# Performance work log

Hardware: AMD Instinct MI355X
Metric: run time of the kernel (lower is better)

## Reference

```python
import jax, jax.numpy as jnp
import numpy as np

VOCAB = 32000
D_MODEL = 1024
BLOCK = 2048
RESIDUAL_SCALE = 0.125
B, T = 2, 2048


def setup_inputs() -> dict:
    key = jax.random.key(0)
    ks = jax.random.split(key, 10)
    s = 0.02
    idx = jax.random.randint(ks[0], (B, T), 0, VOCAB)
    tok_emb = jax.random.normal(ks[1], (VOCAB, D_MODEL), jnp.float32) * s
    pos_emb = jax.random.normal(ks[2], (BLOCK, D_MODEL), jnp.float32) * s
    Wq = jax.random.normal(ks[3], (D_MODEL, D_MODEL), jnp.float32) * s
    Wk = jax.random.normal(ks[4], (D_MODEL, D_MODEL), jnp.float32) * s
    Wv = jax.random.normal(ks[5], (D_MODEL, D_MODEL), jnp.float32) * s
    W1 = jax.random.normal(ks[6], (D_MODEL, 4 * D_MODEL), jnp.float32) * s
    b1 = jnp.zeros((4 * D_MODEL,), jnp.float32)
    W2 = jax.random.normal(ks[7], (4 * D_MODEL, D_MODEL), jnp.float32) * s
    b2 = jnp.zeros((D_MODEL,), jnp.float32)
    Wout = jax.random.normal(ks[8], (D_MODEL, VOCAB), jnp.float32) * s
    bout = jnp.zeros((VOCAB,), jnp.float32)
    return {"idx": idx, "tok_emb": tok_emb, "pos_emb": pos_emb, "Wq": Wq,
            "Wk": Wk, "Wv": Wv, "W1": W1, "b1": b1, "W2": W2, "b2": b2,
            "Wout": Wout, "bout": bout}


def reference(idx, tok_emb, pos_emb, Wq, Wk, Wv, W1, b1, W2, b2, Wout, bout):
    Bc, Tc = idx.shape
    scale = 1.0 / jnp.sqrt(jnp.asarray(D_MODEL, jnp.float32))
    x = tok_emb[idx] + pos_emb[:Tc]                       # [B,T,D]
    q = x @ Wq
    k = x @ Wk
    v = x @ Wv
    scores = jnp.einsum('bqd,bkd->bqk', q, k) * scale     # [B,T,T]
    causal = jnp.tril(jnp.ones((Tc, Tc), bool))
    scores = jnp.where(causal, scores, -jnp.inf)
    attn = jax.nn.softmax(scores, axis=-1)
    attn_out = jnp.einsum('bqk,bkd->bqd', attn, v)
    x = x + RESIDUAL_SCALE * attn_out
    h = jax.nn.gelu(x @ W1 + b1, approximate=False)
    x = x + (h @ W2 + b2)
    return x @ Wout + bout                                 # [B,T,V]
```

## Files before the change

### kernel.cpp

```cpp
#include <hip/hip_runtime.h>
#include <math.h>

typedef unsigned int uint;
typedef unsigned short u16;
typedef __bf16 v8bf __attribute__((ext_vector_type(8)));
typedef float v4f __attribute__((ext_vector_type(4)));

__device__ inline u16 f2b(float f) {
  union { float f; uint u; } c; c.f = f;
  uint u = c.u;
  return (u16)((u + 0x7fffu + ((u >> 16) & 1u)) >> 16);
}

__global__ __launch_bounds__(256) void k_embed(
    const int* __restrict__ idx, const float* __restrict__ tok,
    const float* __restrict__ pos, float* __restrict__ x,
    u16* __restrict__ xb, int T, int D) {
  const int r = blockIdx.x;
  const int t = threadIdx.x;
  const int token = idx[r];
  const int p = r % T;
  const float4 a = ((const float4*)(tok + (size_t)token * D))[t];
  const float4 b = ((const float4*)(pos + (size_t)p * D))[t];
  float4 o;
  o.x = a.x + b.x; o.y = a.y + b.y; o.z = a.z + b.z; o.w = a.w + b.w;
  ((float4*)(x + (size_t)r * D))[t] = o;
  ushort4 ob;
  ob.x = f2b(o.x); ob.y = f2b(o.y); ob.z = f2b(o.z); ob.w = f2b(o.w);
  ((ushort4*)(xb + (size_t)r * D))[t] = ob;
}

__global__ __launch_bounds__(256) void k_castT(
    const float* __restrict__ in, u16* __restrict__ out, int R, int C) {
  __shared__ float tile[32][33];
  const int tx = threadIdx.x & 31, ty = threadIdx.x >> 5;
  const int c0 = blockIdx.x * 32, r0 = blockIdx.y * 32;
  for (int j = ty; j < 32; j += 8)
    tile[j][tx] = in[(size_t)(r0 + j) * C + c0 + tx];
  __syncthreads();
  for (int j = ty; j < 32; j += 8)
    out[(size_t)(c0 + j) * R + r0 + tx] = f2b(tile[tx][j]);
}

__global__ __launch_bounds__(256) void k_softmax(
    const float* __restrict__ scores, u16* __restrict__ probs, int T) {
  const int r = blockIdx.x;
  const int i = r % T;
  const float* srow = scores + (size_t)r * T;
  u16* prow = probs + (size_t)r * T;
  const int t = threadIdx.x;
  const int n = i + 1;
  __shared__ float red[256];
  float mx = -3.0e38f;
  for (int j = t; j < n; j += 256) mx = fmaxf(mx, srow[j]);
  red[t] = mx; __syncthreads();
  for (int s = 128; s > 0; s >>= 1) {
    if (t < s) red[t] = fmaxf(red[t], red[t + s]);
    __syncthreads();
  }
  mx = red[0]; __syncthreads();
  float sum = 0.f;
  for (int j = t; j < n; j += 256) sum += __expf(srow[j] - mx);
  red[t] = sum; __syncthreads();
  for (int s = 128; s > 0; s >>= 1) {
    if (t < s) red[t] += red[t + s];
    __syncthreads();
  }
  const float inv = 1.0f / red[0];
  for (int j = t; j < T; j += 256) {
    float p = (j < n) ? __expf(srow[j] - mx) * inv : 0.0f;
    prow[j] = f2b(p);
  }
}

__global__ __launch_bounds__(256) void k_gemm_nt(
    const u16* __restrict__ A, const u16* __restrict__ B,
    const float* __restrict__ src, const float* __restrict__ bias,
    float* __restrict__ Cf, u16* __restrict__ Cb,
    int M, int N, int K, float alpha, int act, int causal_skip) {
  __shared__ __align__(16) u16 As[128 * 40];
  __shared__ __align__(16) u16 Bs[128 * 40];
  const int t = threadIdx.x;
  const int m0 = blockIdx.y * 128, n0 = blockIdx.x * 128;
  if (causal_skip && n0 > m0 + 127) return;
  const int lane = t & 63, wave = t >> 6;
  const int wm = (wave >> 1) * 64, wn = (wave & 1) * 64;
  const int lm = lane & 15, lq = lane >> 4;

  v4f acc[4][4];
#pragma unroll
  for (int i = 0; i < 4; i++)
#pragma unroll
    for (int j = 0; j < 4; j++)
#pragma unroll
      for (int r = 0; r < 4; r++) acc[i][j][r] = 0.0f;

  const int r0 = t >> 2;
  const int cg = (t & 3) * 8;

  for (int k0 = 0; k0 < K; k0 += 32) {
    {
      const size_t abase = (size_t)(m0 + r0) * K + k0 + cg;
      *(uint4*)&As[r0 * 40 + cg]        = *(const uint4*)&A[abase];
      *(uint4*)&As[(r0 + 64) * 40 + cg] = *(const uint4*)&A[abase + (size_t)64 * K];
      const size_t bbase = (size_t)(n0 + r0) * K + k0 + cg;
      *(uint4*)&Bs[r0 * 40 + cg]        = *(const uint4*)&B[bbase];
      *(uint4*)&Bs[(r0 + 64) * 40 + cg] = *(const uint4*)&B[bbase + (size_t)64 * K];
    }
    __syncthreads();
    v8bf af[4], bf[4];
#pragma unroll
    for (int i = 0; i < 4; i++)
      af[i] = *(const v8bf*)&As[(wm + i * 16 + lm) * 40 + lq * 8];
#pragma unroll
    for (int j = 0; j < 4; j++)
      bf[j] = *(const v8bf*)&Bs[(wn + j * 16 + lm) * 40 + lq * 8];
#pragma unroll
    for (int i = 0; i < 4; i++)
#pragma unroll
      for (int j = 0; j < 4; j++)
        acc[i][j] = __builtin_amdgcn_mfma_f32_16x16x32_bf16(af[i], bf[j], acc[i][j], 0, 0, 0);
    __syncthreads();
  }

#pragma unroll
  for (int i = 0; i < 4; i++) {
#pragma unroll
    for (int j = 0; j < 4; j++) {
      const int col = n0 + wn + j * 16 + lm;
      const float bv = bias ? bias[col] : 0.0f;
      const int rowb = m0 + wm + i * 16 + lq * 4;
#pragma unroll
      for (int r = 0; r < 4; r++) {
        float v = alpha * acc[i][j][r] + bv;
        const size_t off = (size_t)(rowb + r) * N + col;
        if (src) v += src[off];
        if (act) v = 0.5f * v * (1.0f + erff(v * 0.70710678118654752f));
        if (Cf) Cf[off] = v;
        if (Cb) Cb[off] = f2b(v);
      }
    }
  }
}

extern "C" void kernel_launch(void* const* d_in, const int* in_sizes, int n_in,
                              void* d_out, int out_size, void* d_ws, size_t ws_size,
                              hipStream_t stream) {
  (void)in_sizes; (void)n_in; (void)out_size; (void)ws_size;
  const int B = 2, T = 2048, D = 1024, V = 32000, H = 4096, M = B * T;
  const int* idx   = (const int*)d_in[0];
  const float* tok = (const float*)d_in[1];
  const float* pos = (const float*)d_in[2];
  const float* Wq  = (const float*)d_in[3];
  const float* Wk  = (const float*)d_in[4];
  const float* Wv  = (const float*)d_in[5];
  const float* W1  = (const float*)d_in[6];
  const float* b1  = (const float*)d_in[7];
  const float* W2  = (const float*)d_in[8];
  const float* b2  = (const float*)d_in[9];
  const float* Wout = (const float*)d_in[10];
  const float* bout = (const float*)d_in[11];
  float* out = (float*)d_out;

  char* w = (char*)d_ws;
  const size_t MB = 1u << 20;
  float* x      = (float*)(w);
  u16*  xb      = (u16*)(w + 16 * MB);
  u16*  qb      = (u16*)(w + 24 * MB);
  u16*  kb      = (u16*)(w + 32 * MB);
  u16*  vt      = (u16*)(w + 40 * MB);
  float* vf     = (float*)(w + 48 * MB);
  float* x2     = vf;
  float* scores = (float*)(w + 64 * MB);
  u16*  hb      = (u16*)(w + 64 * MB);
  u16*  probs   = (u16*)(w + 96 * MB);
  u16*  x2b     = (u16*)(w + 112 * MB);
  u16*  x3b     = (u16*)(w + 120 * MB);
  u16*  wT      = (u16*)(w + 128 * MB);

  dim3 blk(256);

  k_embed<<<M, blk, 0, stream>>>(idx, tok, pos, x, xb, T, D);

  k_castT<<<dim3(D / 32, D / 32), blk, 0, stream>>>(Wq, wT, D, D);
  k_gemm_nt<<<dim3(D / 128, M / 128), blk, 0, stream>>>(
      xb, wT, nullptr, nullptr, nullptr, qb, M, D, D, 1.0f, 0, 0);
  k_castT<<<dim3(D / 32, D / 32), blk, 0, stream>>>(Wk, wT, D, D);
  k_gemm_nt<<<dim3(D / 128, M / 128), blk, 0, stream>>>(
      xb, wT, nullptr, nullptr, nullptr, kb, M, D, D, 1.0f, 0, 0);
  k_castT<<<dim3(D / 32, D / 32), blk, 0, stream>>>(Wv, wT, D, D);
  k_gemm_nt<<<dim3(D / 128, M / 128), blk, 0, stream>>>(
      xb, wT, nullptr, nullptr, vf, nullptr, M, D, D, 1.0f, 0, 0);

  for (int b = 0; b < B; b++)
    k_castT<<<dim3(D / 32, T / 32), blk, 0, stream>>>(
        vf + (size_t)b * T * D, vt + (size_t)b * D * T, T, D);

  for (int b = 0; b < B; b++)
    k_gemm_nt<<<dim3(T / 128, T / 128), blk, 0, stream>>>(
        qb + (size_t)b * T * D, kb + (size_t)b * T * D, nullptr, nullptr,
        scores + (size_t)b * T * T, nullptr, T, T, D, 1.0f / 32.0f, 0, 1);

  k_softmax<<<B * T, blk, 0, stream>>>(scores, probs, T);

  for (int b = 0; b < B; b++)
    k_gemm_nt<<<dim3(D / 128, T / 128), blk, 0, stream>>>(
        probs + (size_t)b * T * T, vt + (size_t)b * D * T,
        x + (size_t)b * T * D, nullptr,
        x2 + (size_t)b * T * D, x2b + (size_t)b * T * D, T, D, T, 0.125f, 0, 0);

  k_castT<<<dim3(H / 32, D / 32), blk, 0, stream>>>(W1, wT, D, H);
  k_gemm_nt<<<dim3(H / 128, M / 128), blk, 0, stream>>>(
      x2b, wT, nullptr, b1, nullptr, hb, M, H, D, 1.0f, 1, 0);

  k_castT<<<dim3(D / 32, H / 32), blk, 0, stream>>>(W2, wT, H, D);
  k_gemm_nt<<<dim3(D / 128, M / 128), blk, 0, stream>>>(
      hb, wT, x2, b2, nullptr, x3b, M, D, H, 1.0f, 0, 0);

  k_castT<<<dim3(V / 32, D / 32), blk, 0, stream>>>(Wout, wT, D, V);
  k_gemm_nt<<<dim3(V / 128, M / 128), blk, 0, stream>>>(
      x3b, wT, nullptr, bout, out, nullptr, M, V, D, 1.0f, 0, 0);
}
```

Before: 1.566 ms.

## Use direct global-to-LDS loads in GEMM, swizzle block order, register-cache softmax

The GEMM tile loads now use global_load_lds, which writes global data straight into LDS without a pass through registers. To fit that path the LDS padding is removed, so rows go from a 40-element to a 32-element stride. Thread blocks are remapped with an XCD-style interleave for better cache locality across the chiplets. Softmax keeps each row's scores in registers so it reads global memory once, instead of re-reading for max, sum and output. The unpadded LDS layout risks bank conflicts on the fragment reads. The softmax hard-codes 8 chunks of 256 elements, which assumes T is at most 2048.

```diff
diff --git a/kernel.cpp b/kernel.cpp
--- a/kernel.cpp
+++ b/kernel.cpp
@@ -5,6 +5,9 @@
 typedef unsigned short u16;
 typedef __bf16 v8bf __attribute__((ext_vector_type(8)));
 typedef float v4f __attribute__((ext_vector_type(4)));
+
+#define GLP(x) ((const __attribute__((address_space(1))) void*)(x))
+#define LDP(x) ((__attribute__((address_space(3))) void*)(x))
 
 __device__ inline u16 f2b(float f) {
   union { float f; uint u; } c; c.f = f;
@@ -51,8 +54,16 @@
   const int t = threadIdx.x;
   const int n = i + 1;
   __shared__ float red[256];
+
+  float vals[8];
+#pragma unroll
+  for (int c = 0; c < 8; c++) {
+    const int j = t + c * 256;
+    vals[c] = (j < n) ? srow[j] : -3.0e38f;
+  }
   float mx = -3.0e38f;
-  for (int j = t; j < n; j += 256) mx = fmaxf(mx, srow[j]);
+#pragma unroll
+  for (int c = 0; c < 8; c++) mx = fmaxf(mx, vals[c]);
   red[t] = mx; __syncthreads();
   for (int s = 128; s > 0; s >>= 1) {
     if (t < s) red[t] = fmaxf(red[t], red[t + s]);
@@ -60,16 +71,21 @@
   }
   mx = red[0]; __syncthreads();
   float sum = 0.f;
-  for (int j = t; j < n; j += 256) sum += __expf(srow[j] - mx);
+#pragma unroll
+  for (int c = 0; c < 8; c++) {
+    const float e = (t + c * 256 < n) ? __expf(vals[c] - mx) : 0.0f;
+    vals[c] = e; sum += e;
+  }
   red[t] = sum; __syncthreads();
   for (int s = 128; s > 0; s >>= 1) {
     if (t < s) red[t] += red[t + s];
     __syncthreads();
   }
   const float inv = 1.0f / red[0];
-  for (int j = t; j < T; j += 256) {
-    float p = (j < n) ? __expf(srow[j] - mx) * inv : 0.0f;
-    prow[j] = f2b(p);
+#pragma unroll
+  for (int c = 0; c < 8; c++) {
+    const int j = t + c * 256;
+    if (j < T) prow[j] = f2b(vals[c] * inv);
   }
 }
 
@@ -78,11 +94,21 @@
     const float* __restrict__ src, const float* __restrict__ bias,
     float* __restrict__ Cf, u16* __restrict__ Cb,
     int M, int N, int K, float alpha, int act, int causal_skip) {
-  __shared__ __align__(16) u16 As[128 * 40];
-  __shared__ __align__(16) u16 Bs[128 * 40];
+  __shared__ __align__(16) u16 As[128 * 32];
+  __shared__ __align__(16) u16 Bs[128 * 32];
   const int t = threadIdx.x;
-  const int m0 = blockIdx.y * 128, n0 = blockIdx.x * 128;
+
+  int bx = blockIdx.x, by = blockIdx.y;
+  const int nwg = gridDim.x * gridDim.y;
+  if ((nwg & 7) == 0) {
+    int bid = by * gridDim.x + bx;
+    bid = (bid & 7) * (nwg >> 3) + (bid >> 3);
+    bx = bid % gridDim.x;
+    by = bid / gridDim.x;
+  }
+  const int m0 = by * 128, n0 = bx * 128;
   if (causal_skip && n0 > m0 + 127) return;
+
   const int lane = t & 63, wave = t >> 6;
   const int wm = (wave >> 1) * 64, wn = (wave & 1) * 64;
   const int lm = lane & 15, lq = lane >> 4;
@@ -95,31 +121,36 @@
 #pragma unroll
       for (int r = 0; r < 4; r++) acc[i][j][r] = 0.0f;
 
-  const int r0 = t >> 2;
-  const int cg = (t & 3) * 8;
+  const int srow = lane >> 2;
+  const int scol = (lane & 3) * 8;
+  const u16* ag = A + (size_t)(m0 + wave * 32 + srow) * K + scol;
+  const u16* bg = B + (size_t)(n0 + wave * 32 + srow) * K + scol;
+  const size_t rstep = (size_t)16 * K;
+  u16* const la0 = &As[(wave * 32) * 32];
+  u16* const la1 = &As[(wave * 32 + 16) * 32];
+  u16* const lb0 = &Bs[(wave * 32) * 32];
+  u16* const lb1 = &Bs[(wave * 32 + 16) * 32];
 
   for (int k0 = 0; k0 < K; k0 += 32) {
-    {
-      const size_t abase = (size_t)(m0 + r0) * K + k0 + cg;
-      *(uint4*)&As[r0 * 40 + cg]        = *(const uint4*)&A[abase];
-      *(uint4*)&As[(r0 + 64) * 40 + cg] = *(const uint4*)&A[abase + (size_t)64 * K];
-      const size_t bbase = (size_t)(n0 + r0) * K + k0 + cg;
-      *(uint4*)&Bs[r0 * 40 + cg]        = *(const uint4*)&B[bbase];
-      *(uint4*)&Bs[(r0 + 64) * 40 + cg] = *(const uint4*)&B[bbase + (size_t)64 * K];
-    }
-    __syncthreads();
-    v8bf af[4], bf[4];
+    __builtin_amdgcn_global_load_lds(GLP(ag),         LDP(la0), 16, 0, 0);
+    __builtin_amdgcn_global_load_lds(GLP(ag + rstep), LDP(la1), 16, 0, 0);
+    __builtin_amdgcn_global_load_lds(GLP(bg),         LDP(lb0), 16, 0, 0);
+    __builtin_amdgcn_global_load_lds(GLP(bg + rstep), LDP(lb1), 16, 0, 0);
+    ag += 32; bg += 32;
+    __syncthreads();
+
+    v8bf af[4], bfr[4];
 #pragma unroll
     for (int i = 0; i < 4; i++)
-      af[i] = *(const v8bf*)&As[(wm + i * 16 + lm) * 40 + lq * 8];
+      af[i] = *(const v8bf*)&As[(wm + i * 16 + lm) * 32 + lq * 8];
 #pragma unroll
     for (int j = 0; j < 4; j++)
-      bf[j] = *(const v8bf*)&Bs[(wn + j * 16 + lm) * 40 + lq * 8];
+      bfr[j] = *(const v8bf*)&Bs[(wn + j * 16 + lm) * 32 + lq * 8];
 #pragma unroll
     for (int i = 0; i < 4; i++)
 #pragma unroll
       for (int j = 0; j < 4; j++)
-        acc[i][j] = __builtin_amdgcn_mfma_f32_16x16x32_bf16(af[i], bf[j], acc[i][j], 0, 0, 0);
+        acc[i][j] = __builtin_amdgcn_mfma_f32_16x16x32_bf16(af[i], bfr[j], acc[i][j], 0, 0, 0);
     __syncthreads();
   }
 
```

After: 1.547 ms. Within noise of the previous version (-1.2%).
